# Optimization experiments

Hardware: AMD Instinct MI355X
Metric: run time of the kernel (lower is better)

## Reference

```python
import jax, jax.numpy as jnp
import numpy as np

B, T, ENC, DEC, ATTN = 64, 2048, 512, 512, 256


def setup_inputs() -> dict:
    key = jax.random.key(0)
    k1, k2, k3, k4, k5, k6 = jax.random.split(key, 6)
    enc_out = jax.random.normal(k1, (B, T, ENC), dtype=jnp.float32)
    dec_hidden = jax.random.normal(k2, (B, DEC), dtype=jnp.float32)
    mask = jax.random.randint(k3, (B, T), 0, 2) == 1  # True = masked out
    # learned params (Linear with bias=False); torch Linear weight is [out,in],
    # we store transposed [in,out] for x @ W convention
    s_enc = 1.0 / np.sqrt(ENC)
    s_dec = 1.0 / np.sqrt(DEC)
    s_v = 1.0 / np.sqrt(ATTN)
    W_enc = jax.random.uniform(k4, (ENC, ATTN), jnp.float32, -s_enc, s_enc)
    W_dec = jax.random.uniform(k5, (DEC, ATTN), jnp.float32, -s_dec, s_dec)
    v = jax.random.uniform(k6, (ATTN,), jnp.float32, -s_v, s_v)
    return {"enc_out": enc_out, "dec_hidden": dec_hidden, "mask": mask,
            "W_enc": W_enc, "W_dec": W_dec, "v": v}


def reference(enc_out, dec_hidden, mask, W_enc, W_dec, v):
    # proj_enc: [B,T,A]; proj_dec: [B,1,A]
    proj_enc = jnp.einsum('bte,ea->bta', enc_out, W_enc)
    proj_dec = jnp.einsum('bd,da->ba', dec_hidden, W_dec)[:, None, :]
    # energy: [B,T] -- additive (Bahdanau) score
    energy = jnp.einsum('bta,a->bt', jnp.tanh(proj_enc + proj_dec), v)
    energy = jnp.where(mask, -jnp.inf, energy)
    attn_w = jax.nn.softmax(energy, axis=-1)
    attn_w = jnp.nan_to_num(attn_w, nan=0.0)  # fully-masked rows -> 0
    context = jnp.einsum('bt,bte->be', attn_w, enc_out)
    return context, attn_w
```

## Files before the change

### kernel.cpp

```cpp
#include <hip/hip_runtime.h>
#include <stdint.h>

#define Bx 64
#define Tx 2048
#define ENCx 512
#define ATTx 256

typedef float f4 __attribute__((ext_vector_type(4)));
typedef float f32x4 __attribute__((ext_vector_type(4)));
typedef short bf16x8 __attribute__((ext_vector_type(8)));

__device__ __forceinline__ unsigned short f2bf(float f) {
  union { float f; uint32_t u; } c; c.f = f;
  uint32_t u = c.u;
  u += 0x7fffu + ((u >> 16) & 1u);
  return (unsigned short)(u >> 16);
}

__device__ __forceinline__ uint32_t pk_bf(float lo, float hi) {
  uint32_t a = __float_as_uint(lo) + 0x8000u;
  uint32_t b = __float_as_uint(hi) + 0x8000u;
  return __builtin_amdgcn_perm(b, a, 0x07060302u);
}

__device__ __forceinline__ float ftanh(float x) {
  x = fminf(8.f, fmaxf(-8.f, x));
  float z = __expf(2.f * x);
  return 1.f - __fdividef(2.f, z + 1.f);
}

__global__ void k0_wt(const float* __restrict__ W, unsigned short* __restrict__ WTc) {
  int tid = blockIdx.x * 256 + threadIdx.x;
  int kc = tid >> 13;
  int r = tid & 8191;
  int n = r >> 5;
  int kk = r & 31;
  WTc[tid] = f2bf(W[(kc * 32 + kk) * ATTx + n]);
}

__global__ void k1_pd(const float* __restrict__ dec, const float* __restrict__ Wd,
                      float* __restrict__ pd) {
  __shared__ float ld[512];
  int b = blockIdx.x, a = threadIdx.x;
  ld[a] = dec[b * 512 + a];
  ld[a + 256] = dec[b * 512 + a + 256];
  __syncthreads();
  float s = 0.f;
#pragma unroll 8
  for (int d = 0; d < 512; ++d) s = fmaf(ld[d], Wd[d * ATTx + a], s);
  pd[b * ATTx + a] = s;
}

__global__ __launch_bounds__(256, 3) void k2_fused(
    const float* __restrict__ enc, const unsigned short* __restrict__ WTc,
    const float* __restrict__ pd, const float* __restrict__ v,
    const int* __restrict__ mask, float* __restrict__ energy,
    float* __restrict__ part, float* __restrict__ mloc, float* __restrict__ lloc) {
  __shared__ float pdv[256];
  __shared__ float vvs[256];
  __shared__ float e_lds[128];
  __shared__ float wl[128];

  const int tid = threadIdx.x;
  const int wid = tid >> 6;
  const int lane = tid & 63;
  const int q = lane >> 4;
  const int c15 = lane & 15;
  const int m0 = blockIdx.x * 128;
  const int b = m0 >> 11;
  const int chunk = blockIdx.x & 15;

  pdv[tid] = pd[b * ATTx + tid];
  vvs[tid] = v[tid];
  __syncthreads();

  const int mrow = m0 + wid * 32 + c15;
  const float* a0p = enc + (size_t)mrow * ENCx + q * 8;
  const float* a1p = a0p + 16 * ENCx;
  const unsigned short* wb = WTc + c15 * 32 + q * 8;

  f32x4 acc[2][16];
#pragma unroll
  for (int mt = 0; mt < 2; ++mt)
#pragma unroll
    for (int ct = 0; ct < 16; ++ct) { f32x4 z = {0.f,0.f,0.f,0.f}; acc[mt][ct] = z; }

  f4 x0 = *(const f4*)(a0p);
  f4 x1 = *(const f4*)(a0p + 4);
  f4 y0 = *(const f4*)(a1p);
  f4 y1 = *(const f4*)(a1p + 4);

  for (int kc = 0; kc < 16; ++kc) {
    bf16x8 bfr[16];
    const unsigned short* wkc = wb + kc * 8192;
#pragma unroll
    for (int ct = 0; ct < 16; ++ct)
      bfr[ct] = *(const bf16x8*)(wkc + ct * 512);

    const int kn = (kc < 15) ? kc + 1 : 15;
    f4 nx0 = *(const f4*)(a0p + kn * 32);
    f4 nx1 = *(const f4*)(a0p + kn * 32 + 4);
    f4 ny0 = *(const f4*)(a1p + kn * 32);
    f4 ny1 = *(const f4*)(a1p + kn * 32 + 4);

    union { uint32_t u[4]; bf16x8 v; } am0, am1;
    am0.u[0] = pk_bf(x0.x, x0.y); am0.u[1] = pk_bf(x0.z, x0.w);
    am0.u[2] = pk_bf(x1.x, x1.y); am0.u[3] = pk_bf(x1.z, x1.w);
    am1.u[0] = pk_bf(y0.x, y0.y); am1.u[1] = pk_bf(y0.z, y0.w);
    am1.u[2] = pk_bf(y1.x, y1.y); am1.u[3] = pk_bf(y1.z, y1.w);

#pragma unroll
    for (int ct = 0; ct < 16; ++ct) {
      acc[0][ct] = __builtin_amdgcn_mfma_f32_16x16x32_bf16(am0.v, bfr[ct], acc[0][ct], 0, 0, 0);
      acc[1][ct] = __builtin_amdgcn_mfma_f32_16x16x32_bf16(am1.v, bfr[ct], acc[1][ct], 0, 0, 0);
    }
    x0 = nx0; x1 = nx1; y0 = ny0; y1 = ny1;
  }

  float ps[2][4];
#pragma unroll
  for (int mt = 0; mt < 2; ++mt)
#pragma unroll
    for (int i = 0; i < 4; ++i) ps[mt][i] = 0.f;
#pragma unroll
  for (int ct = 0; ct < 16; ++ct) {
    float pv = pdv[ct * 16 + c15];
    float vv = vvs[ct * 16 + c15];
#pragma unroll
    for (int mt = 0; mt < 2; ++mt)
#pragma unroll
      for (int i = 0; i < 4; ++i)
        ps[mt][i] += ftanh(acc[mt][ct][i] + pv) * vv;
  }
#pragma unroll
  for (int s = 1; s < 16; s <<= 1)
#pragma unroll
    for (int mt = 0; mt < 2; ++mt)
#pragma unroll
      for (int i = 0; i < 4; ++i)
        ps[mt][i] += __shfl_xor(ps[mt][i], s, 64);
  if (c15 == 0) {
#pragma unroll
    for (int mt = 0; mt < 2; ++mt)
#pragma unroll
      for (int i = 0; i < 4; ++i) {
        int lr = wid * 32 + mt * 16 + q * 4 + i;
        int gm = m0 + lr;
        float ev = mask[gm] ? -1e30f : ps[mt][i];
        energy[gm] = ev;
        e_lds[lr] = ev;
      }
  }
  __syncthreads();

  float ev0 = e_lds[lane];
  float ev1 = e_lds[lane + 64];
  float mx = fmaxf(ev0, ev1);
#pragma unroll
  for (int s = 1; s < 64; s <<= 1) mx = fmaxf(mx, __shfl_xor(mx, s, 64));
  float w0 = (ev0 < -1e29f) ? 0.f : __expf(ev0 - mx);
  float w1 = (ev1 < -1e29f) ? 0.f : __expf(ev1 - mx);
  float ls = w0 + w1;
#pragma unroll
  for (int s = 1; s < 64; s <<= 1) ls += __shfl_xor(ls, s, 64);
  if (wid == 0) { wl[lane] = w0; wl[lane + 64] = w1; }
  if (tid == 0) { mloc[b * 16 + chunk] = mx; lloc[b * 16 + chunk] = ls; }
  __syncthreads();

  const float2* e2 = (const float2*)(enc + ((size_t)b * Tx + chunk * 128) * ENCx);
  float ax = 0.f, ay = 0.f;
#pragma unroll 4
  for (int t = 0; t < 128; ++t) {
    float wv = wl[t];
    float2 p = e2[(size_t)t * 256 + tid];
    ax = fmaf(p.x, wv, ax);
    ay = fmaf(p.y, wv, ay);
  }
  float2 r; r.x = ax; r.y = ay;
  *(float2*)(part + ((size_t)chunk * 64 + b) * 512 + tid * 2) = r;
}

__global__ void k3_merge(const float* __restrict__ energy, const float* __restrict__ part,
                         const float* __restrict__ mloc, const float* __restrict__ lloc,
                         float* __restrict__ attn, float* __restrict__ ctx) {
  __shared__ float redm[4];
  __shared__ float redl[4];
  __shared__ float sc[16];
  int b = blockIdx.x, tid = threadIdx.x;
  int lane = tid & 63, wid = tid >> 6;

  float e[8];
#pragma unroll
  for (int i = 0; i < 8; ++i) e[i] = energy[b * Tx + tid + i * 256];
  float m = e[0];
#pragma unroll
  for (int i = 1; i < 8; ++i) m = fmaxf(m, e[i]);
#pragma unroll
  for (int s = 1; s < 64; s <<= 1) m = fmaxf(m, __shfl_xor(m, s, 64));
  if (lane == 0) redm[wid] = m;
  __syncthreads();
  m = fmaxf(fmaxf(redm[0], redm[1]), fmaxf(redm[2], redm[3]));
  bool dead = (m < -1e29f);
  float w[8];
  float l = 0.f;
#pragma unroll
  for (int i = 0; i < 8; ++i) { w[i] = dead ? 0.f : __expf(e[i] - m); l += w[i]; }
#pragma unroll
  for (int s = 1; s < 64; s <<= 1) l += __shfl_xor(l, s, 64);
  if (lane == 0) redl[wid] = l;
  __syncthreads();
  l = redl[0] + redl[1] + redl[2] + redl[3];
  float inv = dead ? 0.f : __fdividef(1.f, l);
#pragma unroll
  for (int i = 0; i < 8; ++i) attn[b * Tx + tid + i * 256] = w[i] * inv;

  if (tid < 64) {
    float mc = (lane < 16) ? mloc[b * 16 + lane] : -3e38f;
    float lc = (lane < 16) ? lloc[b * 16 + lane] : 0.f;
    float mg = mc;
#pragma unroll
    for (int s = 1; s < 64; s <<= 1) mg = fmaxf(mg, __shfl_xor(mg, s, 64));
    float sl = (lane < 16) ? lc * __expf(mc - mg) : 0.f;
    float lg = sl;
#pragma unroll
    for (int s = 1; s < 64; s <<= 1) lg += __shfl_xor(lg, s, 64);
    float ig = (lg > 0.f) ? __fdividef(1.f, lg) : 0.f;
    if (lane < 16) sc[lane] = __expf(mc - mg) * ig;
  }
  __syncthreads();
  float2 a; a.x = 0.f; a.y = 0.f;
  const float* pb = part + (size_t)b * 512 + tid * 2;
#pragma unroll 4
  for (int c = 0; c < 16; ++c) {
    float2 p = *(const float2*)(pb + (size_t)c * 32768);
    float s = sc[c];
    a.x = fmaf(p.x, s, a.x);
    a.y = fmaf(p.y, s, a.y);
  }
  *(float2*)(ctx + b * 512 + tid * 2) = a;
}

extern "C" void kernel_launch(void* const* d_in, const int* in_sizes, int n_in,
                              void* d_out, int out_size, void* d_ws, size_t ws_size,
                              hipStream_t stream) {
  const float* enc   = (const float*)d_in[0];
  const float* dec   = (const float*)d_in[1];
  const int*   mask  = (const int*)d_in[2];
  const float* W_enc = (const float*)d_in[3];
  const float* W_dec = (const float*)d_in[4];
  const float* v     = (const float*)d_in[5];
  float* ctx  = (float*)d_out;
  float* attn = ctx + Bx * ENCx;
  char* ws = (char*)d_ws;
  unsigned short* WTc = (unsigned short*)ws;
  float* pd     = (float*)(ws + 262144);
  float* energy = (float*)(ws + 327680);
  float* part   = (float*)(ws + 851968);
  float* mloc   = (float*)(ws + 851968 + 2097152);
  float* lloc   = (float*)(ws + 851968 + 2097152 + 4096);

  k0_wt<<<512, 256, 0, stream>>>(W_enc, WTc);
  k1_pd<<<64, 256, 0, stream>>>(dec, W_dec, pd);
  k2_fused<<<1024, 256, 0, stream>>>(enc, WTc, pd, v, mask, energy, part, mloc, lloc);
  k3_merge<<<64, 256, 0, stream>>>(energy, part, mloc, lloc, attn, ctx);
}
```

Before: 506.6 us.

## Merge prep kernels, split context accumulation across waves, relax launch bounds

Combines the weight-transpose and decoder-projection kernels into one launch to save a kernel launch. In the fused kernel, the context accumulation loop now gives each wave 32 timesteps instead of having every thread walk all 128. Each wave loads four float2 per row, and the four partial sums are reduced through shared memory. The launch-bounds occupancy hint of 3 is dropped, which may change register allocation and occupancy. The extra LDS reduction buffer and the added barrier cost some shared memory and synchronisation.

```diff
diff --git a/kernel.cpp b/kernel.cpp
--- a/kernel.cpp
+++ b/kernel.cpp
@@ -29,29 +29,30 @@
   return 1.f - __fdividef(2.f, z + 1.f);
 }
 
-__global__ void k0_wt(const float* __restrict__ W, unsigned short* __restrict__ WTc) {
-  int tid = blockIdx.x * 256 + threadIdx.x;
-  int kc = tid >> 13;
-  int r = tid & 8191;
-  int n = r >> 5;
-  int kk = r & 31;
-  WTc[tid] = f2bf(W[(kc * 32 + kk) * ATTx + n]);
-}
-
-__global__ void k1_pd(const float* __restrict__ dec, const float* __restrict__ Wd,
-                      float* __restrict__ pd) {
-  __shared__ float ld[512];
-  int b = blockIdx.x, a = threadIdx.x;
-  ld[a] = dec[b * 512 + a];
-  ld[a + 256] = dec[b * 512 + a + 256];
-  __syncthreads();
-  float s = 0.f;
+__global__ void k01_prep(const float* __restrict__ W, unsigned short* __restrict__ WTc,
+                         const float* __restrict__ dec, const float* __restrict__ Wd,
+                         float* __restrict__ pd) {
+  if (blockIdx.x < 512) {
+    int tid = blockIdx.x * 256 + threadIdx.x;
+    int kc = tid >> 13;
+    int r = tid & 8191;
+    int n = r >> 5;
+    int kk = r & 31;
+    WTc[tid] = f2bf(W[(kc * 32 + kk) * ATTx + n]);
+  } else {
+    __shared__ float ld[512];
+    int b = blockIdx.x - 512, a = threadIdx.x;
+    ld[a] = dec[b * 512 + a];
+    ld[a + 256] = dec[b * 512 + a + 256];
+    __syncthreads();
+    float s = 0.f;
 #pragma unroll 8
-  for (int d = 0; d < 512; ++d) s = fmaf(ld[d], Wd[d * ATTx + a], s);
-  pd[b * ATTx + a] = s;
-}
-
-__global__ __launch_bounds__(256, 3) void k2_fused(
+    for (int d = 0; d < 512; ++d) s = fmaf(ld[d], Wd[d * ATTx + a], s);
+    pd[b * ATTx + a] = s;
+  }
+}
+
+__global__ __launch_bounds__(256) void k2_fused(
     const float* __restrict__ enc, const unsigned short* __restrict__ WTc,
     const float* __restrict__ pd, const float* __restrict__ v,
     const int* __restrict__ mask, float* __restrict__ energy,
@@ -60,6 +61,7 @@
   __shared__ float vvs[256];
   __shared__ float e_lds[128];
   __shared__ float wl[128];
+  __shared__ float2 red[4][256];
 
   const int tid = threadIdx.x;
   const int wid = tid >> 6;
@@ -168,15 +170,30 @@
   __syncthreads();
 
   const float2* e2 = (const float2*)(enc + ((size_t)b * Tx + chunk * 128) * ENCx);
-  float ax = 0.f, ay = 0.f;
+  const int t0 = wid * 32;
+  float2 a0; a0.x = 0.f; a0.y = 0.f;
+  float2 a1 = a0, a2 = a0, a3 = a0;
 #pragma unroll 4
-  for (int t = 0; t < 128; ++t) {
-    float wv = wl[t];
-    float2 p = e2[(size_t)t * 256 + tid];
-    ax = fmaf(p.x, wv, ax);
-    ay = fmaf(p.y, wv, ay);
-  }
-  float2 r; r.x = ax; r.y = ay;
+  for (int t = 0; t < 32; ++t) {
+    float wv = wl[t0 + t];
+    const float2* row = e2 + (size_t)(t0 + t) * 256;
+    float2 p0 = row[lane];
+    float2 p1 = row[lane + 64];
+    float2 p2 = row[lane + 128];
+    float2 p3 = row[lane + 192];
+    a0.x = fmaf(p0.x, wv, a0.x); a0.y = fmaf(p0.y, wv, a0.y);
+    a1.x = fmaf(p1.x, wv, a1.x); a1.y = fmaf(p1.y, wv, a1.y);
+    a2.x = fmaf(p2.x, wv, a2.x); a2.y = fmaf(p2.y, wv, a2.y);
+    a3.x = fmaf(p3.x, wv, a3.x); a3.y = fmaf(p3.y, wv, a3.y);
+  }
+  red[wid][lane] = a0;
+  red[wid][lane + 64] = a1;
+  red[wid][lane + 128] = a2;
+  red[wid][lane + 192] = a3;
+  __syncthreads();
+
+  float2 r0 = red[0][tid], r1 = red[1][tid], r2 = red[2][tid], r3 = red[3][tid];
+  float2 r; r.x = (r0.x + r1.x) + (r2.x + r3.x); r.y = (r0.y + r1.y) + (r2.y + r3.y);
   *(float2*)(part + ((size_t)chunk * 64 + b) * 512 + tid * 2) = r;
 }
 
@@ -259,8 +276,7 @@
   float* mloc   = (float*)(ws + 851968 + 2097152);
   float* lloc   = (float*)(ws + 851968 + 2097152 + 4096);
 
-  k0_wt<<<512, 256, 0, stream>>>(W_enc, WTc);
-  k1_pd<<<64, 256, 0, stream>>>(dec, W_dec, pd);
+  k01_prep<<<576, 256, 0, stream>>>(W_enc, WTc, dec, W_dec, pd);
   k2_fused<<<1024, 256, 0, stream>>>(enc, WTc, pd, v, mask, energy, part, mloc, lloc);
   k3_merge<<<64, 256, 0, stream>>>(energy, part, mloc, lloc, attn, ctx);
 }
```

Measured after the change: 477.9 us. 5.7% less time.
